# Optimization experiments

Measured on AMD Instinct MI355X. Metric: run time of the kernel, lower is better.

The kernel has to match this reference:

```python
import jax, jax.numpy as jnp
import numpy as np

CUBE_LEN = 512
EQU_H = 1024
EQU_W = 2 * EQU_H
EQU_COUNT = 4
CHANNELS = 3


def _rodrigues(r):
    th = np.linalg.norm(r)
    if th < 1e-12:
        return np.eye(3)
    k = r / th
    K = np.array([[0.0, -k[2], k[1]], [k[2], 0.0, -k[0]], [-k[1], k[0], 0.0]])
    return np.eye(3) + np.sin(th) * K + (1.0 - np.cos(th)) * (K @ K)


def _build_lut(L, equ_h):
    # Identical math to Cube2Equirec.__init__/_intersection, fused into
    # per-pixel face id + per-pixel cube-face pixel coordinates (u, v).
    equ_w = equ_h * 2
    theta = (np.arange(equ_w) / (equ_w - 1) - 0.5) * 2 * np.pi
    phi = (np.arange(equ_h) / (equ_h - 1) - 0.5) * np.pi
    theta, phi = np.meshgrid(theta, phi)
    x = np.sin(theta) * np.cos(phi)
    y = np.sin(phi)
    z = np.cos(theta) * np.cos(phi)
    xyz = np.stack([x, y, z], axis=-1)  # [H, W, 3]
    planes = np.array([[0, 0, 1, -1], [1, 0, 0, -1], [0, 0, 1, 1],
                       [1, 0, 0, 1], [0, 1, 0, 1], [0, 1, 0, -1]], dtype=np.float64)
    r_lst = np.array([[0, 0, 0], [0, -0.5, 0], [0, 1, 0],
                      [0, 0.5, 0], [-0.5, 0, 0], [0.5, 0, 0]]) * np.pi
    f = L / 2.0
    K = np.array([[f, 0, (L - 1) / 2.0], [0, f, (L - 1) / 2.0], [0, 0, 1]])
    R_lst = np.stack([_rodrigues(r) for r in r_lst])  # [6, 3, 3]

    abc = planes[:, :3]
    with np.errstate(divide='ignore'):
        depth = -planes[:, 3][None, None, :] / (xyz @ abc.T)  # [H, W, 6]
    depth[depth < 0] = np.inf
    arg = np.argmin(depth, axis=-1)            # per-pixel face id
    dmin = np.min(depth, axis=-1)
    pts = dmin[..., None] * xyz                # intersection points
    Rs = R_lst[arg]                            # [H, W, 3, 3]
    proj = np.einsum('ij,hwjk,hwk->hwi', K, Rs, pts)  # K @ R @ pts
    uv = np.clip(proj[..., :2] / proj[..., 2:3], 0, L - 1)
    return uv.astype(np.float32), arg.astype(np.int32)


def setup_inputs() -> dict:
    key = jax.random.key(0)
    x = jax.random.normal(key, (6 * EQU_COUNT, CHANNELS, CUBE_LEN, CUBE_LEN),
                          dtype=jnp.float32)
    uv_np, face_np = _build_lut(CUBE_LEN, EQU_H)
    return {"x": x, "uv": jnp.asarray(uv_np), "face_idx": jnp.asarray(face_np)}


def _cube2equirec(x, uv, face_idx):
    # x: [6*E, C, L, L]; grid_sample(mode='bilinear', align_corners=True)
    # with grid = (uv/(L-1) - 0.5)*2 samples exactly at pixel coords uv.
    E6, C, L, _ = x.shape
    E = E6 // 6
    xr = x.reshape(E, 6, C, L, L)
    H, W = face_idx.shape
    f = face_idx.reshape(-1)                 # [N]
    u = uv[..., 0].reshape(-1)               # [N], in [0, L-1]
    v = uv[..., 1].reshape(-1)

    x0 = jnp.clip(jnp.floor(u).astype(jnp.int32), 0, L - 1)
    y0 = jnp.clip(jnp.floor(v).astype(jnp.int32), 0, L - 1)
    x1 = jnp.minimum(x0 + 1, L - 1)
    y1 = jnp.minimum(y0 + 1, L - 1)
    wx = (u - x0.astype(u.dtype))[:, None, None]  # [N,1,1]
    wy = (v - y0.astype(v.dtype))[:, None, None]

    def g(yy, xx):
        # advanced indices at axes 1,3,4 -> result [N, E, C]
        return xr[:, f, :, yy, xx]

    out = (g(y0, x0) * (1 - wx) * (1 - wy)
           + g(y0, x1) * wx * (1 - wy)
           + g(y1, x0) * (1 - wx) * wy
           + g(y1, x1) * wx * wy)              # [N, E, C]
    return jnp.transpose(out, (1, 2, 0)).reshape(E, C, H, W)


def reference(x, uv, face_idx):
    return _cube2equirec(x, uv, face_idx)
```

## Files before the change

### kernel.cpp

```cpp
#include <hip/hip_runtime.h>

#define CUBE_LEN   512
#define EQU_H      1024
#define EQU_W      2048
#define EQU_COUNT  4
#define CHANNELS   3

__global__ __launch_bounds__(256, 1) void cube2equirec_kernel(
    const float* __restrict__ x,
    const float* __restrict__ uv,
    const int*   __restrict__ face,
    float*       __restrict__ out)
{
    const int HW  = EQU_H * EQU_W;
    const int idx = blockIdx.x * blockDim.x + threadIdx.x;
    if (idx >= HW) return;

    const float2 uvv = ((const float2*)uv)[idx];
    const float u = uvv.x;
    const float v = uvv.y;
    const int   f = face[idx];

    int x0 = (int)floorf(u);
    int y0 = (int)floorf(v);
    x0 = min(max(x0, 0), CUBE_LEN - 2);
    y0 = min(max(y0, 0), CUBE_LEN - 2);

    const float wx = u - (float)x0;
    const float wy = v - (float)y0;

    const int o00 = y0 * CUBE_LEN + x0;
    const int o10 = o00 + CUBE_LEN;

    const int PLANE = CUBE_LEN * CUBE_LEN;
    const int IMG   = CHANNELS * PLANE;

    float a00[EQU_COUNT * CHANNELS], a01[EQU_COUNT * CHANNELS];
    float a10[EQU_COUNT * CHANNELS], a11[EQU_COUNT * CHANNELS];
#pragma unroll
    for (int e = 0; e < EQU_COUNT; ++e) {
        const int img_base = (e * 6 + f) * IMG;
#pragma unroll
        for (int c = 0; c < CHANNELS; ++c) {
            const float* __restrict__ p = x + img_base + c * PLANE;
            const int i = e * CHANNELS + c;
            a00[i] = p[o00];
            a01[i] = p[o00 + 1];
            a10[i] = p[o10];
            a11[i] = p[o10 + 1];
        }
    }

    __builtin_amdgcn_sched_barrier(0);

    const float w00 = (1.0f - wx) * (1.0f - wy);
    const float w01 = wx * (1.0f - wy);
    const float w10 = (1.0f - wx) * wy;
    const float w11 = wx * wy;

#pragma unroll
    for (int i = 0; i < EQU_COUNT * CHANNELS; ++i) {
        const float val = a00[i] * w00 + a01[i] * w01
                        + a10[i] * w10 + a11[i] * w11;
        __builtin_nontemporal_store(val, &out[i * HW + idx]);
    }
}

extern "C" void kernel_launch(void* const* d_in, const int* in_sizes, int n_in,
                              void* d_out, int out_size, void* d_ws, size_t ws_size,
                              hipStream_t stream) {
    const float* x    = (const float*)d_in[0];
    const float* uv   = (const float*)d_in[1];
    const int*   face = (const int*)d_in[2];
    float*       out  = (float*)d_out;

    const int HW = EQU_H * EQU_W;
    const int block = 256;
    const int grid  = (HW + block - 1) / block;

    hipLaunchKernelGGL(cube2equirec_kernel, dim3(grid), dim3(block), 0, stream,
                       x, uv, face, out);
}
```

Baseline: 220.0 us.

## Process two pixels per thread with shared 4-wide vector gathers via inline asm

Each thread now handles two adjacent output pixels. When both pixels hit the same face and row with nearby x, it fetches a single dwordx4 pair per channel image and derives both bilinear results from it, using per-slot weight vectors. Otherwise it falls back to extra dwordx2 loads for the second pixel. Loads are issued as inline asm using scalar base addresses and are batched six images per round, and stores become 2-wide nontemporal writes. This cuts gather instruction count and address arithmetic, at the cost of hand-written asm, divergence on the non-compatible path, and a full vmcnt(0) wait per round.

```diff
diff --git a/kernel.cpp b/kernel.cpp
--- a/kernel.cpp
+++ b/kernel.cpp
@@ -1,69 +1,159 @@
 #include <hip/hip_runtime.h>
+#include <stdint.h>
 
 #define CUBE_LEN   512
 #define EQU_H      1024
 #define EQU_W      2048
 #define EQU_COUNT  4
 #define CHANNELS   3
+#define HW         (EQU_H * EQU_W)
 
-__global__ __launch_bounds__(256, 1) void cube2equirec_kernel(
+typedef float f32x4 __attribute__((ext_vector_type(4)));
+typedef float f32x2 __attribute__((ext_vector_type(2)));
+
+#define IMG_OFF(i) ((uint64_t)(((i) / 3) * 18874368u + ((i) % 3) * 1048576u))
+
+__global__ __launch_bounds__(128, 1) void cube2equirec_kernel(
     const float* __restrict__ x,
     const float* __restrict__ uv,
     const int*   __restrict__ face,
     float*       __restrict__ out)
 {
-    const int HW  = EQU_H * EQU_W;
-    const int idx = blockIdx.x * blockDim.x + threadIdx.x;
-    if (idx >= HW) return;
+    const int tid = blockIdx.x * 128 + threadIdx.x;
 
-    const float2 uvv = ((const float2*)uv)[idx];
-    const float u = uvv.x;
-    const float v = uvv.y;
-    const int   f = face[idx];
+    const f32x4 uv4 = ((const f32x4*)uv)[tid];
+    const int2  fpr = ((const int2*)face)[tid];
+    const float uA = uv4.x, vA = uv4.y, uB = uv4.z, vB = uv4.w;
+    const int   fA = fpr.x, fB = fpr.y;
 
-    int x0 = (int)floorf(u);
-    int y0 = (int)floorf(v);
-    x0 = min(max(x0, 0), CUBE_LEN - 2);
-    y0 = min(max(y0, 0), CUBE_LEN - 2);
+    int x0A = (int)floorf(uA), y0A = (int)floorf(vA);
+    int x0B = (int)floorf(uB), y0B = (int)floorf(vB);
+    x0A = min(max(x0A, 0), 510); y0A = min(max(y0A, 0), 510);
+    x0B = min(max(x0B, 0), 510); y0B = min(max(y0B, 0), 510);
+    const float wxA = uA - (float)x0A, wyA = vA - (float)y0A;
+    const float wxB = uB - (float)x0B, wyB = vB - (float)y0B;
 
-    const float wx = u - (float)x0;
-    const float wy = v - (float)y0;
+    const int  xmw    = min(x0A, x0B);
+    const bool compat = (fA == fB) && (y0A == y0B)
+                     && ((max(x0A, x0B) - xmw) <= 2);
+    const int xm = min(compat ? xmw : x0A, 508);
+    const int oA = x0A - xm;
+    const int oB = min(max(x0B - xm, 0), 2);
 
-    const int o00 = y0 * CUBE_LEN + x0;
-    const int o10 = o00 + CUBE_LEN;
+    const uint32_t vbW = (uint32_t)(fA * 3145728 + y0A * 2048 + xm * 4);
+    const uint32_t vbB = (uint32_t)(fB * 3145728 + y0B * 2048 + x0B * 4);
+    const uint64_t xb  = (uint64_t)x;
 
-    const int PLANE = CUBE_LEN * CUBE_LEN;
-    const int IMG   = CHANNELS * PLANE;
+    const float aL = 1.f - wxA, aR = wxA;
+    const float bL = 1.f - wxB, bR = wxB;
+    f32x4 WA, WB;
+    WA.x = (oA == 0) ? aL : 0.f;
+    WA.y = (oA == 0) ? aR : ((oA == 1) ? aL : 0.f);
+    WA.z = (oA == 2) ? aL : ((oA == 1) ? aR : 0.f);
+    WA.w = (oA == 2) ? aR : 0.f;
+    WB.x = (oB == 0) ? bL : 0.f;
+    WB.y = (oB == 0) ? bR : ((oB == 1) ? bL : 0.f);
+    WB.z = (oB == 2) ? bL : ((oB == 1) ? bR : 0.f);
+    WB.w = (oB == 2) ? bR : 0.f;
+    const f32x4 WA0 = WA * (1.f - wyA), WA1 = WA * wyA;
+    const f32x4 WB0 = WB * (1.f - wyB), WB1 = WB * wyB;
+    const float c00 = bL * (1.f - wyB), c01 = bR * (1.f - wyB);
+    const float c10 = bL * wyB,         c11 = bR * wyB;
 
-    float a00[EQU_COUNT * CHANNELS], a01[EQU_COUNT * CHANNELS];
-    float a10[EQU_COUNT * CHANNELS], a11[EQU_COUNT * CHANNELS];
-#pragma unroll
-    for (int e = 0; e < EQU_COUNT; ++e) {
-        const int img_base = (e * 6 + f) * IMG;
-#pragma unroll
-        for (int c = 0; c < CHANNELS; ++c) {
-            const float* __restrict__ p = x + img_base + c * PLANE;
-            const int i = e * CHANNELS + c;
-            a00[i] = p[o00];
-            a01[i] = p[o00 + 1];
-            a10[i] = p[o10];
-            a11[i] = p[o10 + 1];
-        }
+#define EMIT2(i, R0, R1, Q0, Q1)                                             \
+    {                                                                        \
+        const float ovA = R0.x * WA0.x + R0.y * WA0.y + R0.z * WA0.z         \
+                        + R0.w * WA0.w + R1.x * WA1.x + R1.y * WA1.y         \
+                        + R1.z * WA1.z + R1.w * WA1.w;                       \
+        const float oBw = R0.x * WB0.x + R0.y * WB0.y + R0.z * WB0.z         \
+                        + R0.w * WB0.w + R1.x * WB1.x + R1.y * WB1.y         \
+                        + R1.z * WB1.z + R1.w * WB1.w;                       \
+        const float oBf = Q0.x * c00 + Q0.y * c01 + Q1.x * c10 + Q1.y * c11; \
+        f32x2 st;                                                            \
+        st.x = ovA;                                                          \
+        st.y = compat ? oBw : oBf;                                           \
+        __builtin_nontemporal_store(st, (f32x2*)(out + (size_t)(i) * HW) + tid); \
     }
 
-    __builtin_amdgcn_sched_barrier(0);
+#define ROUND(I0)                                                            \
+    {                                                                        \
+        f32x4 r0_0, r1_0, r0_1, r1_1, r0_2, r1_2,                            \
+              r0_3, r1_3, r0_4, r1_4, r0_5, r1_5;                            \
+        asm volatile(                                                        \
+            "global_load_dwordx4 %[a0], %[vb], %[s0]\n\t"                    \
+            "global_load_dwordx4 %[b0], %[vb], %[s0] offset:2048\n\t"        \
+            "global_load_dwordx4 %[a1], %[vb], %[s1]\n\t"                    \
+            "global_load_dwordx4 %[b1], %[vb], %[s1] offset:2048\n\t"        \
+            "global_load_dwordx4 %[a2], %[vb], %[s2]\n\t"                    \
+            "global_load_dwordx4 %[b2], %[vb], %[s2] offset:2048\n\t"        \
+            "global_load_dwordx4 %[a3], %[vb], %[s3]\n\t"                    \
+            "global_load_dwordx4 %[b3], %[vb], %[s3] offset:2048\n\t"        \
+            "global_load_dwordx4 %[a4], %[vb], %[s4]\n\t"                    \
+            "global_load_dwordx4 %[b4], %[vb], %[s4] offset:2048\n\t"        \
+            "global_load_dwordx4 %[a5], %[vb], %[s5]\n\t"                    \
+            "global_load_dwordx4 %[b5], %[vb], %[s5] offset:2048"            \
+            : [a0] "=&v"(r0_0), [b0] "=&v"(r1_0),                            \
+              [a1] "=&v"(r0_1), [b1] "=&v"(r1_1),                            \
+              [a2] "=&v"(r0_2), [b2] "=&v"(r1_2),                            \
+              [a3] "=&v"(r0_3), [b3] "=&v"(r1_3),                            \
+              [a4] "=&v"(r0_4), [b4] "=&v"(r1_4),                            \
+              [a5] "=&v"(r0_5), [b5] "=&v"(r1_5)                             \
+            : [vb] "v"(vbW),                                                 \
+              [s0] "s"(xb + IMG_OFF((I0) + 0)),                              \
+              [s1] "s"(xb + IMG_OFF((I0) + 1)),                              \
+              [s2] "s"(xb + IMG_OFF((I0) + 2)),                              \
+              [s3] "s"(xb + IMG_OFF((I0) + 3)),                              \
+              [s4] "s"(xb + IMG_OFF((I0) + 4)),                              \
+              [s5] "s"(xb + IMG_OFF((I0) + 5)));                             \
+        f32x2 q0_0 = {0.f, 0.f}, q1_0 = {0.f, 0.f};                          \
+        f32x2 q0_1 = {0.f, 0.f}, q1_1 = {0.f, 0.f};                          \
+        f32x2 q0_2 = {0.f, 0.f}, q1_2 = {0.f, 0.f};                          \
+        f32x2 q0_3 = {0.f, 0.f}, q1_3 = {0.f, 0.f};                          \
+        f32x2 q0_4 = {0.f, 0.f}, q1_4 = {0.f, 0.f};                          \
+        f32x2 q0_5 = {0.f, 0.f}, q1_5 = {0.f, 0.f};                          \
+        if (!compat) {                                                       \
+            asm volatile(                                                    \
+                "global_load_dwordx2 %[a0], %[vb], %[s0]\n\t"                \
+                "global_load_dwordx2 %[b0], %[vb], %[s0] offset:2048\n\t"    \
+                "global_load_dwordx2 %[a1], %[vb], %[s1]\n\t"                \
+                "global_load_dwordx2 %[b1], %[vb], %[s1] offset:2048\n\t"    \
+                "global_load_dwordx2 %[a2], %[vb], %[s2]\n\t"                \
+                "global_load_dwordx2 %[b2], %[vb], %[s2] offset:2048\n\t"    \
+                "global_load_dwordx2 %[a3], %[vb], %[s3]\n\t"                \
+                "global_load_dwordx2 %[b3], %[vb], %[s3] offset:2048\n\t"    \
+                "global_load_dwordx2 %[a4], %[vb], %[s4]\n\t"                \
+                "global_load_dwordx2 %[b4], %[vb], %[s4] offset:2048\n\t"    \
+                "global_load_dwordx2 %[a5], %[vb], %[s5]\n\t"                \
+                "global_load_dwordx2 %[b5], %[vb], %[s5] offset:2048"        \
+                : [a0] "=&v"(q0_0), [b0] "=&v"(q1_0),                        \
+                  [a1] "=&v"(q0_1), [b1] "=&v"(q1_1),                        \
+                  [a2] "=&v"(q0_2), [b2] "=&v"(q1_2),                        \
+                  [a3] "=&v"(q0_3), [b3] "=&v"(q1_3),                        \
+                  [a4] "=&v"(q0_4), [b4] "=&v"(q1_4),                        \
+                  [a5] "=&v"(q0_5), [b5] "=&v"(q1_5)                         \
+                : [vb] "v"(vbB),                                             \
+                  [s0] "s"(xb + IMG_OFF((I0) + 0)),                          \
+                  [s1] "s"(xb + IMG_OFF((I0) + 1)),                          \
+                  [s2] "s"(xb + IMG_OFF((I0) + 2)),                          \
+                  [s3] "s"(xb + IMG_OFF((I0) + 3)),                          \
+                  [s4] "s"(xb + IMG_OFF((I0) + 4)),                          \
+                  [s5] "s"(xb + IMG_OFF((I0) + 5)));                         \
+        }                                                                    \
+        asm volatile("s_waitcnt vmcnt(0)" ::: "memory");                     \
+        __builtin_amdgcn_sched_barrier(0);                                   \
+        EMIT2((I0) + 0, r0_0, r1_0, q0_0, q1_0)                              \
+        EMIT2((I0) + 1, r0_1, r1_1, q0_1, q1_1)                              \
+        EMIT2((I0) + 2, r0_2, r1_2, q0_2, q1_2)                              \
+        EMIT2((I0) + 3, r0_3, r1_3, q0_3, q1_3)                              \
+        EMIT2((I0) + 4, r0_4, r1_4, q0_4, q1_4)                              \
+        EMIT2((I0) + 5, r0_5, r1_5, q0_5, q1_5)                              \
+    }
 
-    const float w00 = (1.0f - wx) * (1.0f - wy);
-    const float w01 = wx * (1.0f - wy);
-    const float w10 = (1.0f - wx) * wy;
-    const float w11 = wx * wy;
+    ROUND(0)
+    ROUND(6)
 
-#pragma unroll
-    for (int i = 0; i < EQU_COUNT * CHANNELS; ++i) {
-        const float val = a00[i] * w00 + a01[i] * w01
-                        + a10[i] * w10 + a11[i] * w11;
-        __builtin_nontemporal_store(val, &out[i * HW + idx]);
-    }
+#undef ROUND
+#undef EMIT2
 }
 
 extern "C" void kernel_launch(void* const* d_in, const int* in_sizes, int n_in,
@@ -74,10 +164,7 @@
     const int*   face = (const int*)d_in[2];
     float*       out  = (float*)d_out;
 
-    const int HW = EQU_H * EQU_W;
-    const int block = 256;
-    const int grid  = (HW + block - 1) / block;
-
-    hipLaunchKernelGGL(cube2equirec_kernel, dim3(grid), dim3(block), 0, stream,
+    const int grid = (HW / 2) / 128;
+    hipLaunchKernelGGL(cube2equirec_kernel, dim3(grid), dim3(128), 0, stream,
                        x, uv, face, out);
 }
```

Measured after the change: 224.3 us. Within noise of the previous version (+2.0%).
